# Kernel tuning notes

Measured on AMD Instinct MI355X. Metric: run time of the kernel, lower is better.

## Reference

```python
import jax, jax.numpy as jnp
import numpy as np

DECAY = 0.1
EPS = 1e-5


def setup_inputs() -> dict:
    key = jax.random.key(0)
    k1, k2, k3 = jax.random.split(key, 3)
    H, N, D, K = 1, 32768, 256, 4096
    x = jax.random.normal(k1, (H, N, D), dtype=jnp.float32)
    embed = jax.random.normal(k2, (H, K, D), dtype=jnp.float32) * 0.01
    cluster_size = jnp.ones((H, K), dtype=jnp.float32)
    embed_avg = jax.random.normal(k3, (H, K, D), dtype=jnp.float32) * 0.01
    return {"x": x, "embed": embed, "cluster_size": cluster_size, "embed_avg": embed_avg}


def reference(x, embed, cluster_size, embed_avg):
    # x: [H, N, D] flattened latents; embed: [H, K, D] codebook
    H, N, D = x.shape
    K = embed.shape[1]

    x_sq = jnp.sum(x * x, axis=-1, keepdims=True)          # [H, N, 1]
    e_sq = jnp.sum(embed * embed, axis=-1)[:, None, :]     # [H, 1, K]
    dist = x_sq - 2.0 * jnp.einsum('hnd,hkd->hnk', x, embed) + e_sq

    embed_ind = jnp.argmin(dist, axis=-1)                  # [H, N] int

    # gather nearest code vectors: [H, N, D]
    quantize = jax.vmap(lambda e, i: e[i])(embed, embed_ind)

    # EMA statistics (no_grad in torch): bincount + scatter-add of latents
    bins = jax.vmap(lambda i: jax.ops.segment_sum(jnp.ones((N,), x.dtype), i, num_segments=K))(embed_ind)                      # [H, K]
    embed_sum = jax.vmap(lambda xh, ih: jax.ops.segment_sum(xh, ih, num_segments=K))(x, embed_ind)                             # [H, K, D]

    new_cluster_size = cluster_size * DECAY + bins * (1.0 - DECAY)
    new_embed_avg = embed_avg * DECAY + embed_sum * (1.0 - DECAY)

    # laplace-smoothed normalization of codebook
    n = jnp.sum(new_cluster_size, axis=-1, keepdims=True)
    smoothed = (new_cluster_size + EPS) / (n + K * EPS) * n
    embed_normalized = new_embed_avg / smoothed[..., None]  # [H, K, D]

    # commitment loss (quantize detached) and straight-through output
    commit_loss = jnp.mean((jax.lax.stop_gradient(quantize) - x) ** 2)
    out = x + jax.lax.stop_gradient(quantize - x)

    return out, commit_loss, embed_ind, new_cluster_size, embed_normalized
```

## Files before the change

### kernel.cpp

```cpp
#include <hip/hip_runtime.h>
#include <hip/hip_bf16.h>
#include <cstdint>
#include <cstddef>

#define NROWS 32768
#define DDIM 256
#define KCODES 4096

typedef __attribute__((ext_vector_type(8))) short s16x8;
typedef __attribute__((ext_vector_type(4))) float f32x4;
typedef unsigned long long u64;
typedef unsigned int u32;

#define WS_LOSS 0
#define WS_CNT 1
#define WS_EMAX 2
#define WS_DISTRUST 3
#define WS_NSC 4
#define WS_HIST 8
#define WS_OFFS 4104
#define WS_CURSOR 8200
#define WS_LPART 12296
#define WS_RLIST 16392
#define WS_ESUM 49160
#define WS_XSQ 1097736
#define WS_ESQ 1130504
#define WS_IDX 1134600
#define WS_KEY 1167368
#define WS_TKEY 1232904
#define WS_TM2 1757192
#define WS_LIST 2019336
#define WS_EH 2052104
#define WS_EL 2576392
#define WS_TOTAL 3100680
#define WS_ZERO_FLOATS 12296

__device__ __forceinline__ float hsum16_np(const float a[16]) {
    float t3[8];
#pragma unroll
    for (int m = 0; m < 8; ++m) t3[m] = __fadd_rn(a[m + 8], a[m]);
    float t6[4];
#pragma unroll
    for (int m = 0; m < 4; ++m) t6[m] = __fadd_rn(t3[m + 4], t3[m]);
    return __fadd_rn(__fadd_rn(t6[0], t6[2]), __fadd_rn(t6[1], t6[3]));
}

__device__ __forceinline__ float np_sum_sq_128(const float* a) {
    float t[16];
#pragma unroll
    for (int l = 0; l < 16; ++l) {
        float m0 = __fmul_rn(a[l], a[l]);
        float m1 = __fmul_rn(a[16 + l], a[16 + l]);
        float m2 = __fmul_rn(a[32 + l], a[32 + l]);
        float m3 = __fmul_rn(a[48 + l], a[48 + l]);
        float m4 = __fmul_rn(a[64 + l], a[64 + l]);
        float m5 = __fmul_rn(a[80 + l], a[80 + l]);
        float m6 = __fmul_rn(a[96 + l], a[96 + l]);
        float m7 = __fmul_rn(a[112 + l], a[112 + l]);
        float s01 = __fadd_rn(m0, m1);
        float s23 = __fadd_rn(m2, m3);
        float s45 = __fadd_rn(m4, m5);
        float s67 = __fadd_rn(m6, m7);
        t[l] = __fadd_rn(__fadd_rn(s01, s23), __fadd_rn(s45, s67));
    }
    return hsum16_np(t);
}

__global__ void k_rownorm(const float* __restrict__ src, float* __restrict__ dst, int rows) {
    int r = blockIdx.x * blockDim.x + threadIdx.x;
    if (r < rows) {
        const float* p = src + ((size_t)r << 8);
        dst[r] = __fadd_rn(np_sum_sq_128(p), np_sum_sq_128(p + 128));
    }
}

__global__ void k_emax(const float* __restrict__ esq, float* __restrict__ emax) {
    __shared__ float s[1024];
    int t = threadIdx.x;
    float m = 0.0f;
    for (int i = t; i < KCODES; i += 1024) m = fmaxf(m, esq[i]);
    s[t] = m;
    __syncthreads();
    for (int w = 512; w > 0; w >>= 1) {
        if (t < w) s[t] = fmaxf(s[t], s[t + w]);
        __syncthreads();
    }
    if (t == 0) emax[0] = s[0];
}

__device__ __forceinline__ ushort bf16_rn(float x) {
    u32 u = __float_as_uint(x);
    u32 r = (u + 0x7fffu + ((u >> 16) & 1u)) >> 16;
    return (ushort)r;
}
__device__ __forceinline__ float bf16_f(ushort h) { return __uint_as_float(((u32)h) << 16); }

__global__ void k_pack(const float* __restrict__ src, ushort* __restrict__ hi,
                       ushort* __restrict__ lo) {
    int i = (blockIdx.x * 256 + threadIdx.x) * 8;
    float4 v0 = *reinterpret_cast<const float4*>(src + i);
    float4 v1 = *reinterpret_cast<const float4*>(src + i + 4);
    float f[8] = {v0.x, v0.y, v0.z, v0.w, v1.x, v1.y, v1.z, v1.w};
    ushort h[8], l[8];
#pragma unroll
    for (int j = 0; j < 8; ++j) {
        h[j] = bf16_rn(f[j]);
        l[j] = bf16_rn(__fsub_rn(f[j], bf16_f(h[j])));
    }
    *reinterpret_cast<s16x8*>(hi + i) = *reinterpret_cast<s16x8*>(h);
    *reinterpret_cast<s16x8*>(lo + i) = *reinterpret_cast<s16x8*>(l);
}

__device__ __forceinline__ float keyval_(u64 k) {
    u32 u = (u32)(k >> 32);
    u = (u & 0x80000000u) ? (u ^ 0x80000000u) : ~u;
    return __uint_as_float(u);
}
__device__ __forceinline__ u64 packkey(float d, u32 j) {
    u32 u = __float_as_uint(d);
    u ^= (u32)((int)u >> 31) | 0x80000000u;
    return ((u64)u << 32) | j;
}
#define KEY_INIT 0xFF8000007FFFFFFFull

__device__ __forceinline__ void dma16(const void* g, void* l) {
    __builtin_amdgcn_global_load_lds(
        (const __attribute__((address_space(1))) void*)g,
        (__attribute__((address_space(3))) void*)l, 16, 0, 0);
}

__global__ __attribute__((amdgpu_flat_work_group_size(512, 512), amdgpu_waves_per_eu(4, 4)))
void k_mfma(const ushort* __restrict__ xh_g, const ushort* __restrict__ xl_g,
            const ushort* __restrict__ eh_g, const ushort* __restrict__ el_g,
            const float* __restrict__ xsq, const float* __restrict__ esq,
            u64* __restrict__ tkey, float* __restrict__ tm2) {
    __shared__ __align__(16) ushort xh_s[16384];
    __shared__ __align__(16) ushort xl_s[16384];
    __shared__ __align__(16) ushort eh_s[4096];
    __shared__ __align__(16) ushort el_s[4096];

    const int tid = threadIdx.x;
    const int w = tid >> 6, l = tid & 63, lr = l & 15, lg = l >> 4;
    const int lid = blockIdx.x;
    const int xcd = lid & 7, sslot = lid >> 3, sp = sslot >> 3, ww = sslot & 7;
    const int bxg = xcd * 16 + (sp & 3) * 4 + (ww & 3);
    const int jb = ((sp >> 2) << 1) + (ww >> 2);
    const int n0 = bxg * 256, j0 = jb * 512;
    const int key = (lr & 7) << 4;

    float xq[8];
#pragma unroll
    for (int i = 0; i < 8; ++i)
        xq[i] = xsq[n0 + w * 32 + (i >> 2) * 16 + lg * 4 + (i & 3)];

    u64 K1[8];
    float M2[8];
#pragma unroll
    for (int i = 0; i < 8; ++i) { K1[i] = KEY_INIT; M2[i] = __uint_as_float(0x7F800000u); }

    for (int js = 0; js < 8; ++js) {
        const int jbase = j0 + js * 64;
        f32x4 acc[2][4];
#pragma unroll
        for (int a = 0; a < 2; ++a)
#pragma unroll
            for (int b = 0; b < 4; ++b) acc[a][b] = (f32x4){0.f, 0.f, 0.f, 0.f};

        for (int c = 0; c < 4; ++c) {
            __syncthreads();
#pragma unroll
            for (int p = 0; p < 4; ++p) {
                int m = tid + p * 512, r = m >> 3, cb = (m & 7) << 4;
                int so = (n0 + r) * 256 + c * 64 + ((cb ^ ((r & 7) << 4)) >> 1);
                dma16(xh_g + so, (char*)xh_s + m * 16);
                dma16(xl_g + so, (char*)xl_s + m * 16);
            }
            {
                int m = tid, r = m >> 3, cb = (m & 7) << 4;
                int so = (jbase + r) * 256 + c * 64 + ((cb ^ ((r & 7) << 4)) >> 1);
                dma16(eh_g + so, (char*)eh_s + m * 16);
                dma16(el_g + so, (char*)el_s + m * 16);
            }
            __syncthreads();
#pragma unroll
            for (int ks = 0; ks < 2; ++ks) {
                const int off = (ks * 64 + lg * 16) ^ key;
                s16x8 axh[2], axl[2];
#pragma unroll
                for (int ns = 0; ns < 2; ++ns) {
                    const int row = w * 32 + ns * 16 + lr;
                    axh[ns] = *(const s16x8*)((const char*)(xh_s + row * 64) + off);
                    axl[ns] = *(const s16x8*)((const char*)(xl_s + row * 64) + off);
                }
#pragma unroll
                for (int jp = 0; jp < 2; ++jp) {
                    s16x8 beh[2], bel[2];
#pragma unroll
                    for (int q = 0; q < 2; ++q) {
                        const int row = (jp * 2 + q) * 16 + lr;
                        beh[q] = *(const s16x8*)((const char*)(eh_s + row * 64) + off);
                        bel[q] = *(const s16x8*)((const char*)(el_s + row * 64) + off);
                    }
#pragma unroll
                    for (int q = 0; q < 2; ++q) {
                        const int jsub = jp * 2 + q;
#pragma unroll
                        for (int ns = 0; ns < 2; ++ns) {
                            acc[ns][jsub] = __builtin_amdgcn_mfma_f32_16x16x32_bf16(
                                axh[ns], beh[q], acc[ns][jsub], 0, 0, 0);
                            acc[ns][jsub] = __builtin_amdgcn_mfma_f32_16x16x32_bf16(
                                axh[ns], bel[q], acc[ns][jsub], 0, 0, 0);
                            acc[ns][jsub] = __builtin_amdgcn_mfma_f32_16x16x32_bf16(
                                axl[ns], beh[q], acc[ns][jsub], 0, 0, 0);
                        }
                    }
                }
            }
        }
#pragma unroll
        for (int jsub = 0; jsub < 4; ++jsub) {
            const int j = jbase + jsub * 16 + lr;
            const float eq = esq[j];
#pragma unroll
            for (int ns = 0; ns < 2; ++ns)
#pragma unroll
                for (int r = 0; r < 4; ++r) {
                    const float s = acc[ns][jsub][r];
                    const float d = __fadd_rn(__fsub_rn(xq[ns * 4 + r], __fmul_rn(2.0f, s)), eq);
                    const u64 kk = packkey(d, (u32)j);
                    const int i8 = ns * 4 + r;
                    if (kk < K1[i8]) { M2[i8] = keyval_(K1[i8]); K1[i8] = kk; }
                    else if (d < M2[i8]) M2[i8] = d;
                }
        }
    }
#pragma unroll
    for (int i8 = 0; i8 < 8; ++i8) {
        u64 k1 = K1[i8];
        float m2 = M2[i8];
#pragma unroll
        for (int mk = 1; mk < 16; mk <<= 1) {
            u32 klo = __shfl_xor((u32)k1, mk);
            u32 khi = __shfl_xor((u32)(k1 >> 32), mk);
            float om2 = __shfl_xor(m2, mk);
            u64 ok = ((u64)khi << 32) | klo;
            if (ok < k1) { m2 = fminf(om2, keyval_(k1)); k1 = ok; }
            else m2 = fminf(m2, keyval_(ok));
        }
        if (lr == 0) {
            const int n = n0 + w * 32 + (i8 >> 2) * 16 + lg * 4 + (i8 & 3);
            tkey[(size_t)jb * NROWS + n] = k1;
            tm2[(size_t)jb * NROWS + n] = m2;
        }
    }
}

__global__ void k_merge(const u64* __restrict__ tkey, const float* __restrict__ tm2,
                        const float* __restrict__ xsq, const float* __restrict__ emaxp,
                        u64* __restrict__ key64, u32* __restrict__ list, u32* __restrict__ cnt) {
    const int n = blockIdx.x * 256 + threadIdx.x;
    u64 k1 = tkey[n];
    float m2 = tm2[n];
#pragma unroll
    for (int jb = 1; jb < 8; ++jb) {
        u64 ok = tkey[(size_t)jb * NROWS + n];
        float om2 = tm2[(size_t)jb * NROWS + n];
        if (ok < k1) { m2 = fminf(om2, keyval_(k1)); k1 = ok; }
        else m2 = fminf(m2, keyval_(ok));
    }
    const float B = sqrtf(xsq[n] * emaxp[0]);
    const float Ed = 2.4e-4f * B + 1.5e-4f;
    if (m2 - keyval_(k1) <= 2.0f * Ed) {
        key64[n] = ~0ull;
        list[atomicAdd(cnt, 1u)] = (u32)n;
    } else {
        key64[n] = k1;
    }
}

__global__ void k_verify(const float* __restrict__ x, const float* __restrict__ e,
                         const float* __restrict__ xsq, const float* __restrict__ esq,
                         const float* __restrict__ emaxp, u64* __restrict__ key64,
                         u32* __restrict__ list, u32* __restrict__ cnt,
                         u32* __restrict__ distrust) {
    const int li = threadIdx.x & 15;
    const int n = blockIdx.x * 16 + (threadIdx.x >> 4);
    const u64 k = key64[n];
    const bool active = (k != ~0ull);
    const int idx = active ? (int)(k & 0xFFFu) : 0;
    const float* xr = x + ((size_t)n << 8);
    const float* er = e + ((size_t)idx << 8);
    float a = 0.0f;
#pragma unroll
    for (int g = 0; g < 4; ++g)
#pragma unroll
        for (int bb = 3; bb >= 0; --bb) {
            const int d = (g * 4 + bb) * 16 + li;
            a = __builtin_fmaf(xr[d], er[d], a);
        }
    const float s1 = __fadd_rn(__shfl_xor(a, 8), a);
    const float s2 = __fadd_rn(__shfl_xor(s1, 4), s1);
    const float u = __fadd_rn(s2, __shfl_xor(s2, 2));
    const float dot = __fadd_rn(u, __shfl_xor(u, 1));
    if (li == 0 && active) {
        const float d = __fadd_rn(__fsub_rn(xsq[n], __fmul_rn(2.0f, dot)), esq[idx]);
        const float dref = keyval_(k);
        const float B = sqrtf(xsq[n] * emaxp[0]);
        const float Ed = 2.4e-4f * B + 1.5e-4f;
        const float diff = fabsf(d - dref);
        if (diff > Ed) {
            key64[n] = ~0ull;
            list[atomicAdd(cnt, 1u)] = (u32)n;
            if (diff > 0.05f) atomicOr(distrust, 1u);
        }
    }
}

__global__ void k_distrust(const u32* __restrict__ distrust, u64* __restrict__ key64,
                           u32* __restrict__ list, u32* __restrict__ cnt) {
    if (*distrust == 0u) return;
    const int n = blockIdx.x * 256 + threadIdx.x;
    key64[n] = ~0ull;
    list[n] = (u32)n;
    if (n == 0) *cnt = (u32)NROWS;
}

__global__ __attribute__((amdgpu_flat_work_group_size(512, 512), amdgpu_waves_per_eu(4)))
void k_exact(const float* __restrict__ x, const float* __restrict__ embed,
             const float* __restrict__ xsq, const float* __restrict__ esq,
             const u32* __restrict__ list, const u32* __restrict__ cntp,
             u64* __restrict__ key64) {
    const u32 cnt = *cntp;
    const int grp = blockIdx.x >> 3, seg = blockIdx.x & 7;
    const u32 base = (u32)grp * 32u;
    if (base >= cnt) return;

    __shared__ float xs[32][260];
    __shared__ float es[64][68];
    u64* red = (u64*)&es[0][0];

    const int tid = threadIdx.x;
    const int lane = tid & 63;
    const int w = tid >> 6;
    const int g = w >> 2;
    const int tc = lane & 15;
    const int tr = ((w & 3) << 2) + (lane >> 4);
    const int cbase = (g << 5) + tc;

#pragma unroll
    for (int p = 0; p < 4; ++p) {
        int v = tid + p * 512;
        int r = v >> 6;
        int c4 = (v & 63) << 2;
        u32 row = list[(base + (u32)r < cnt) ? base + r : base];
        const float4 f = *reinterpret_cast<const float4*>(x + ((size_t)row << 8) + c4);
        *reinterpret_cast<float4*>(&xs[r][c4]) = f;
    }

    const u32 row0 = list[(base + (u32)tr < cnt) ? base + tr : base];
    const u32 row1 = list[(base + (u32)tr + 16u < cnt) ? base + tr + 16 : base];
    const float xq0 = xsq[row0];
    const float xq1 = xsq[row1];

    u64 best0 = ~0ull, best1 = ~0ull;

    for (int ktl = 0; ktl < 8; ++ktl) {
        const int k0 = seg * 512 + ktl * 64;
        float acc[2][2][16];
#pragma unroll
        for (int i = 0; i < 2; ++i)
#pragma unroll
            for (int j = 0; j < 2; ++j)
#pragma unroll
                for (int q = 0; q < 16; ++q) acc[i][j][q] = 0.0f;

        for (int c = 0; c < 4; ++c) {
            __syncthreads();
#pragma unroll
            for (int p = 0; p < 2; ++p) {
                int v = tid + p * 512;
                int r = v >> 4;
                int c4 = (v & 15) << 2;
                const float4 f = *reinterpret_cast<const float4*>(
                    embed + ((size_t)(k0 + r) << 8) + (c << 6) + c4);
                *reinterpret_cast<float4*>(&es[r][c4]) = f;
            }
            __syncthreads();
#pragma unroll
            for (int jj = 3; jj >= 0; --jj) {
#pragma unroll
                for (int q = 0; q < 4; ++q) {
                    const int dl = ((c * 4 + jj) << 4) + (q << 2);
                    const int el = (jj << 4) + (q << 2);
                    const float4 a0 = *reinterpret_cast<const float4*>(&xs[tr][dl]);
                    const float4 a1 = *reinterpret_cast<const float4*>(&xs[tr + 16][dl]);
                    const int lb = q << 2;
#pragma unroll
                    for (int j2 = 0; j2 < 2; ++j2) {
                        const float4 b = *reinterpret_cast<const float4*>(&es[cbase + 16 * j2][el]);
                        acc[0][j2][lb + 0] = __builtin_fmaf(a0.x, b.x, acc[0][j2][lb + 0]);
                        acc[0][j2][lb + 1] = __builtin_fmaf(a0.y, b.y, acc[0][j2][lb + 1]);
                        acc[0][j2][lb + 2] = __builtin_fmaf(a0.z, b.z, acc[0][j2][lb + 2]);
                        acc[0][j2][lb + 3] = __builtin_fmaf(a0.w, b.w, acc[0][j2][lb + 3]);
                        acc[1][j2][lb + 0] = __builtin_fmaf(a1.x, b.x, acc[1][j2][lb + 0]);
                        acc[1][j2][lb + 1] = __builtin_fmaf(a1.y, b.y, acc[1][j2][lb + 1]);
                        acc[1][j2][lb + 2] = __builtin_fmaf(a1.z, b.z, acc[1][j2][lb + 2]);
                        acc[1][j2][lb + 3] = __builtin_fmaf(a1.w, b.w, acc[1][j2][lb + 3]);
                    }
                }
            }
        }
#pragma unroll
        for (int j2 = 0; j2 < 2; ++j2) {
            const int kk = k0 + cbase + 16 * j2;
            const float eq = esq[kk];
            {
                const float dist = __fadd_rn(__fsub_rn(xq0, __fmul_rn(2.0f, hsum16_np(acc[0][j2]))), eq);
                const u64 kkey = packkey(dist, (u32)kk);
                best0 = kkey < best0 ? kkey : best0;
            }
            {
                const float dist = __fadd_rn(__fsub_rn(xq1, __fmul_rn(2.0f, hsum16_np(acc[1][j2]))), eq);
                const u64 kkey = packkey(dist, (u32)kk);
                best1 = kkey < best1 ? kkey : best1;
            }
        }
    }

    __syncthreads();
    red[tr * 32 + (g << 4) + tc] = best0;
    red[(tr + 16) * 32 + (g << 4) + tc] = best1;
    __syncthreads();
    if (tid < 32) {
        u64 m = red[tid * 32];
#pragma unroll
        for (int t = 1; t < 32; ++t) {
            u64 v = red[tid * 32 + t];
            m = v < m ? v : m;
        }
        if (base + (u32)tid < cnt) atomicMin(&key64[list[base + tid]], m);
    }
}

__global__ void k_finhist(const u64* __restrict__ key64, int* __restrict__ idx,
                          u32* __restrict__ hist, float* __restrict__ ind_out) {
    const int n = blockIdx.x * 256 + threadIdx.x;
    const int k = (int)(key64[n] & 0xFFFull);
    idx[n] = k;
    atomicAdd(&hist[k], 1u);
    ind_out[n] = (float)k;
}

__global__ void k_histidx(const int* __restrict__ idx, u32* __restrict__ hist,
                          float* __restrict__ ind_out) {
    const int n = blockIdx.x * 256 + threadIdx.x;
    const int k = idx[n];
    atomicAdd(&hist[k], 1u);
    ind_out[n] = (float)k;
}

__global__ __attribute__((amdgpu_flat_work_group_size(512, 512), amdgpu_waves_per_eu(4)))
void k_argmin_full(const float* __restrict__ x, const float* __restrict__ embed,
                   const float* __restrict__ xsq, const float* __restrict__ esq,
                   int* __restrict__ out_idx) {
    __shared__ float xs[32][260];
    __shared__ float es[64][68];
    u64* red = (u64*)&es[0][0];
    const int tid = threadIdx.x;
    const int lane = tid & 63;
    const int w = tid >> 6;
    const int g = w >> 2;
    const int tc = lane & 15;
    const int tr = ((w & 3) << 2) + (lane >> 4);
    const int cbase = (g << 5) + tc;
    const int n0 = blockIdx.x * 32;
#pragma unroll
    for (int p = 0; p < 4; ++p) {
        int v = tid + p * 512;
        int r = v >> 6;
        int c4 = (v & 63) << 2;
        const float4 f = *reinterpret_cast<const float4*>(x + ((size_t)(n0 + r) << 8) + c4);
        *reinterpret_cast<float4*>(&xs[r][c4]) = f;
    }
    const float xq0 = xsq[n0 + tr];
    const float xq1 = xsq[n0 + tr + 16];
    u64 best0 = ~0ull, best1 = ~0ull;
    for (int kt = 0; kt < KCODES / 64; ++kt) {
        const int k0 = kt * 64;
        float acc[2][2][16];
#pragma unroll
        for (int i = 0; i < 2; ++i)
#pragma unroll
            for (int j = 0; j < 2; ++j)
#pragma unroll
                for (int q = 0; q < 16; ++q) acc[i][j][q] = 0.0f;
        for (int c = 0; c < 4; ++c) {
            __syncthreads();
#pragma unroll
            for (int p = 0; p < 2; ++p) {
                int v = tid + p * 512;
                int r = v >> 4;
                int c4 = (v & 15) << 2;
                const float4 f = *reinterpret_cast<const float4*>(
                    embed + ((size_t)(k0 + r) << 8) + (c << 6) + c4);
                *reinterpret_cast<float4*>(&es[r][c4]) = f;
            }
            __syncthreads();
#pragma unroll
            for (int jj = 3; jj >= 0; --jj) {
#pragma unroll
                for (int q = 0; q < 4; ++q) {
                    const int dl = ((c * 4 + jj) << 4) + (q << 2);
                    const int el = (jj << 4) + (q << 2);
                    const float4 a0 = *reinterpret_cast<const float4*>(&xs[tr][dl]);
                    const float4 a1 = *reinterpret_cast<const float4*>(&xs[tr + 16][dl]);
                    const int lb = q << 2;
#pragma unroll
                    for (int j2 = 0; j2 < 2; ++j2) {
                        const float4 b = *reinterpret_cast<const float4*>(&es[cbase + 16 * j2][el]);
                        acc[0][j2][lb + 0] = __builtin_fmaf(a0.x, b.x, acc[0][j2][lb + 0]);
                        acc[0][j2][lb + 1] = __builtin_fmaf(a0.y, b.y, acc[0][j2][lb + 1]);
                        acc[0][j2][lb + 2] = __builtin_fmaf(a0.z, b.z, acc[0][j2][lb + 2]);
                        acc[0][j2][lb + 3] = __builtin_fmaf(a0.w, b.w, acc[0][j2][lb + 3]);
                        acc[1][j2][lb + 0] = __builtin_fmaf(a1.x, b.x, acc[1][j2][lb + 0]);
                        acc[1][j2][lb + 1] = __builtin_fmaf(a1.y, b.y, acc[1][j2][lb + 1]);
                        acc[1][j2][lb + 2] = __builtin_fmaf(a1.z, b.z, acc[1][j2][lb + 2]);
                        acc[1][j2][lb + 3] = __builtin_fmaf(a1.w, b.w, acc[1][j2][lb + 3]);
                    }
                }
            }
        }
#pragma unroll
        for (int j2 = 0; j2 < 2; ++j2) {
            const int kk = k0 + cbase + 16 * j2;
            const float eq = esq[kk];
            {
                const float dist = __fadd_rn(__fsub_rn(xq0, __fmul_rn(2.0f, hsum16_np(acc[0][j2]))), eq);
                const u64 kkey = packkey(dist, (u32)kk);
                best0 = kkey < best0 ? kkey : best0;
            }
            {
                const float dist = __fadd_rn(__fsub_rn(xq1, __fmul_rn(2.0f, hsum16_np(acc[1][j2]))), eq);
                const u64 kkey = packkey(dist, (u32)kk);
                best1 = kkey < best1 ? kkey : best1;
            }
        }
    }
    __syncthreads();
    red[tr * 32 + (g << 4) + tc] = best0;
    red[(tr + 16) * 32 + (g << 4) + tc] = best1;
    __syncthreads();
    if (tid < 32) {
        u64 m = red[tid * 32];
#pragma unroll
        for (int t = 1; t < 32; ++t) {
            u64 v = red[tid * 32 + t];
            m = v < m ? v : m;
        }
        out_idx[n0 + tid] = (int)(m & 0xFFFFFFFFu);
    }
}

__global__ void k_scancluster(const u32* __restrict__ hist, u32* __restrict__ offs,
                              const float* __restrict__ cs, float* __restrict__ ncs_out,
                              float* __restrict__ n_out) {
    __shared__ u32 ts[1024];
    __shared__ float fs[1024];
    const int t = threadIdx.x;
    const u32 h0 = hist[t * 4], h1 = hist[t * 4 + 1], h2 = hist[t * 4 + 2], h3 = hist[t * 4 + 3];
    const u32 tot = h0 + h1 + h2 + h3;
    ts[t] = tot;
    const float n0_ = __fadd_rn(__fmul_rn(cs[t * 4 + 0], 0.1f), __fmul_rn((float)h0, 0.9f));
    const float n1_ = __fadd_rn(__fmul_rn(cs[t * 4 + 1], 0.1f), __fmul_rn((float)h1, 0.9f));
    const float n2_ = __fadd_rn(__fmul_rn(cs[t * 4 + 2], 0.1f), __fmul_rn((float)h2, 0.9f));
    const float n3_ = __fadd_rn(__fmul_rn(cs[t * 4 + 3], 0.1f), __fmul_rn((float)h3, 0.9f));
    ncs_out[t * 4 + 0] = n0_;
    ncs_out[t * 4 + 1] = n1_;
    ncs_out[t * 4 + 2] = n2_;
    ncs_out[t * 4 + 3] = n3_;
    fs[t] = ((n0_ + n1_) + n2_) + n3_;
    __syncthreads();
    for (int o = 1; o < 1024; o <<= 1) {
        const u32 add = (t >= o) ? ts[t - o] : 0u;
        __syncthreads();
        ts[t] += add;
        __syncthreads();
    }
    const u32 excl = ts[t] - tot;
    offs[t * 4] = excl;
    offs[t * 4 + 1] = excl + h0;
    offs[t * 4 + 2] = excl + h0 + h1;
    offs[t * 4 + 3] = excl + h0 + h1 + h2;
    for (int wd = 512; wd > 0; wd >>= 1) {
        if (t < wd) fs[t] += fs[t + wd];
        __syncthreads();
    }
    if (t == 0) n_out[0] = fs[0];
}

__global__ void k_place(const int* __restrict__ idx, u32* __restrict__ cursor,
                        const u32* __restrict__ offs, u32* __restrict__ rlist) {
    const int n = blockIdx.x * 256 + threadIdx.x;
    const int k = idx[n];
    const u32 p = atomicAdd(&cursor[k], 1u);
    rlist[offs[k] + p] = (u32)n;
}

__global__ void k_esum(const float* __restrict__ x, const u32* __restrict__ rlist,
                       const u32* __restrict__ offs, const u32* __restrict__ hist,
                       float* __restrict__ esum) {
    const int k = blockIdx.x;
    const int d = threadIdx.x;
    const u32 o = offs[k], c = hist[k];
    float s = 0.0f;
    for (u32 i = 0; i < c; ++i) s += x[((size_t)rlist[o + i] << 8) + d];
    esum[((size_t)k << 8) + d] = s;
}

__global__ void k_outloss(const float* __restrict__ x, const float* __restrict__ e,
                          const int* __restrict__ idx, float* __restrict__ out,
                          float* __restrict__ lpart) {
    const int d = threadIdx.x;
    float ls = 0.0f;
#pragma unroll
    for (int r = 0; r < 8; ++r) {
        const int n = blockIdx.x * 8 + r;
        const int k = idx[n];
        const size_t xi = ((size_t)n << 8) + d;
        const float xv = x[xi];
        const float qv = e[((size_t)k << 8) + d];
        const float diff = __fsub_rn(qv, xv);
        out[xi] = __fadd_rn(xv, diff);
        ls = __builtin_fmaf(diff, diff, ls);
    }
    __shared__ float sred[256];
    sred[d] = ls;
    __syncthreads();
    for (int s = 128; s > 0; s >>= 1) {
        if (d < s) sred[d] += sred[d + s];
        __syncthreads();
    }
    if (d == 0) lpart[blockIdx.x] = sred[0];
}

__global__ void k_norm(const float* __restrict__ ea, const float* __restrict__ esum,
                       const float* __restrict__ ncs, const float* __restrict__ nptr,
                       float* __restrict__ en_out) {
    const int i = blockIdx.x * 256 + threadIdx.x;
    const int k = i >> 8;
    const float n = nptr[0];
    const float ncsk = ncs[k];
    const float smoothed = (ncsk + 1e-5f) / (n + 4096.0f * 1e-5f) * n;
    const float nea = __fadd_rn(__fmul_rn(ea[i], 0.1f), __fmul_rn(esum[i], 0.9f));
    en_out[i] = nea / smoothed;
}

__global__ void k_loss(const float* __restrict__ lpart, float* __restrict__ dst) {
    __shared__ float s[256];
    const int t = threadIdx.x;
    float a = 0.0f;
    for (int i = t; i < 4096; i += 256) a += lpart[i];
    s[t] = a;
    __syncthreads();
    for (int w = 128; w > 0; w >>= 1) {
        if (t < w) s[t] += s[t + w];
        __syncthreads();
    }
    if (t == 0) dst[0] = s[0] * (1.0f / 8388608.0f);
}

extern "C" void kernel_launch(void* const* d_in, const int* in_sizes, int n_in, void* d_out,
                              int out_size, void* d_ws, size_t ws_size, hipStream_t stream) {
    (void)in_sizes; (void)n_in; (void)out_size;
    const float* x = (const float*)d_in[0];
    const float* emb = (const float*)d_in[1];
    const float* cs = (const float*)d_in[2];
    const float* ea = (const float*)d_in[3];
    float* ws = (float*)d_ws;
    float* out = (float*)d_out;

    u32* w_cnt = (u32*)(ws + WS_CNT);
    float* w_emax = ws + WS_EMAX;
    u32* w_dis = (u32*)(ws + WS_DISTRUST);
    float* w_n = ws + WS_NSC;
    u32* w_hist = (u32*)(ws + WS_HIST);
    u32* w_offs = (u32*)(ws + WS_OFFS);
    u32* w_cursor = (u32*)(ws + WS_CURSOR);
    float* w_lpart = ws + WS_LPART;
    u32* w_rlist = (u32*)(ws + WS_RLIST);
    float* w_esum = ws + WS_ESUM;
    float* w_xsq = ws + WS_XSQ;
    float* w_esq = ws + WS_ESQ;
    int* w_idx = (int*)(ws + WS_IDX);
    u64* w_key = (u64*)(ws + WS_KEY);
    u64* w_tkey = (u64*)(ws + WS_TKEY);
    float* w_tm2 = ws + WS_TM2;
    u32* w_list = (u32*)(ws + WS_LIST);
    ushort* eh_g = (ushort*)(ws + WS_EH);
    ushort* el_g = (ushort*)(ws + WS_EL);

    float* o_out = out;
    float* o_loss = out + 8388608;
    float* o_ind = out + 8388609;
    float* o_ncs = out + 8421377;
    float* o_en = out + 8425473;

    ushort* xh_g = (ushort*)o_out;
    ushort* xl_g = (ushort*)o_out + 8388608;

    hipMemsetAsync(d_ws, 0, (size_t)WS_ZERO_FLOATS * sizeof(float), stream);

    k_rownorm<<<NROWS / 256, 256, 0, stream>>>(x, w_xsq, NROWS);
    k_rownorm<<<KCODES / 256, 256, 0, stream>>>(emb, w_esq, KCODES);

    if (ws_size >= (size_t)WS_TOTAL * sizeof(float)) {
        k_emax<<<1, 1024, 0, stream>>>(w_esq, w_emax);
        k_pack<<<4096, 256, 0, stream>>>(x, xh_g, xl_g);
        k_pack<<<512, 256, 0, stream>>>(emb, eh_g, el_g);
        k_mfma<<<1024, 512, 0, stream>>>(xh_g, xl_g, eh_g, el_g, w_xsq, w_esq,
                                         w_tkey, w_tm2);
        k_merge<<<128, 256, 0, stream>>>(w_tkey, w_tm2, w_xsq, w_emax, w_key, w_list, w_cnt);
        k_verify<<<2048, 256, 0, stream>>>(x, emb, w_xsq, w_esq, w_emax, w_key, w_list,
                                           w_cnt, w_dis);
        k_distrust<<<128, 256, 0, stream>>>(w_dis, w_key, w_list, w_cnt);
        k_exact<<<8192, 512, 0, stream>>>(x, emb, w_xsq, w_esq, w_list, w_cnt, w_key);
        k_finhist<<<128, 256, 0, stream>>>(w_key, w_idx, w_hist, o_ind);
    } else {
        k_argmin_full<<<NROWS / 32, 512, 0, stream>>>(x, emb, w_xsq, w_esq, w_idx);
        k_histidx<<<128, 256, 0, stream>>>(w_idx, w_hist, o_ind);
    }

    k_scancluster<<<1, 1024, 0, stream>>>(w_hist, w_offs, cs, o_ncs, w_n);
    k_place<<<128, 256, 0, stream>>>(w_idx, w_cursor, w_offs, w_rlist);
    k_esum<<<KCODES, 256, 0, stream>>>(x, w_rlist, w_offs, w_hist, w_esum);
    k_outloss<<<NROWS / 8, 256, 0, stream>>>(x, emb, w_idx, o_out, w_lpart);
    k_norm<<<(KCODES * DDIM) / 256, 256, 0, stream>>>(ea, w_esum, o_ncs, w_n, o_en);
    k_loss<<<1, 256, 0, stream>>>(w_lpart, o_loss);
}
```

Measured before the change: 448.2 us.

## Fuse row norms into bf16 packing and esum with normalization; simplify MFMA grid

Row-norm computation is folded into the bf16 hi/lo packing kernel. The codebook max norm is now taken with an atomicMax on the float bits inside that kernel, so the separate rownorm and emax launches go away. Embed-sum accumulation is fused with the EMA/laplace normalization, so the intermediate esum array is neither written nor re-read. The MFMA launch drops its XCD-aware block swizzle for a plain 2D grid, which may change L2 locality across XCDs.

```diff
diff --git a/kernel.cpp b/kernel.cpp
--- a/kernel.cpp
+++ b/kernel.cpp
@@ -32,7 +32,7 @@
 #define WS_LIST 2019336
 #define WS_EH 2052104
 #define WS_EL 2576392
-#define WS_TOTAL 3100680
+#define WS_TOTAL 3055624
 #define WS_ZERO_FLOATS 12296
 
 __device__ __forceinline__ float hsum16_np(const float a[16]) {
@@ -74,20 +74,6 @@
     }
 }
 
-__global__ void k_emax(const float* __restrict__ esq, float* __restrict__ emax) {
-    __shared__ float s[1024];
-    int t = threadIdx.x;
-    float m = 0.0f;
-    for (int i = t; i < KCODES; i += 1024) m = fmaxf(m, esq[i]);
-    s[t] = m;
-    __syncthreads();
-    for (int w = 512; w > 0; w >>= 1) {
-        if (t < w) s[t] = fmaxf(s[t], s[t + w]);
-        __syncthreads();
-    }
-    if (t == 0) emax[0] = s[0];
-}
-
 __device__ __forceinline__ ushort bf16_rn(float x) {
     u32 u = __float_as_uint(x);
     u32 r = (u + 0x7fffu + ((u >> 16) & 1u)) >> 16;
@@ -95,20 +81,41 @@
 }
 __device__ __forceinline__ float bf16_f(ushort h) { return __uint_as_float(((u32)h) << 16); }
 
-__global__ void k_pack(const float* __restrict__ src, ushort* __restrict__ hi,
-                       ushort* __restrict__ lo) {
-    int i = (blockIdx.x * 256 + threadIdx.x) * 8;
-    float4 v0 = *reinterpret_cast<const float4*>(src + i);
-    float4 v1 = *reinterpret_cast<const float4*>(src + i + 4);
+__global__ void k_packnorm(const float* __restrict__ src, ushort* __restrict__ hi,
+                           ushort* __restrict__ lo, float* __restrict__ dst,
+                           u32* __restrict__ emax_u32) {
+    __shared__ float lf[8][257];
+    __shared__ float lsq[8];
+    const int t = threadIdx.x;
+    const int r8 = t >> 5, c8 = (t & 31) << 3;
+    const size_t base = ((size_t)(blockIdx.x * 8 + r8) << 8) + c8;
+    float4 v0 = *reinterpret_cast<const float4*>(src + base);
+    float4 v1 = *reinterpret_cast<const float4*>(src + base + 4);
     float f[8] = {v0.x, v0.y, v0.z, v0.w, v1.x, v1.y, v1.z, v1.w};
     ushort h[8], l[8];
 #pragma unroll
     for (int j = 0; j < 8; ++j) {
         h[j] = bf16_rn(f[j]);
         l[j] = bf16_rn(__fsub_rn(f[j], bf16_f(h[j])));
-    }
-    *reinterpret_cast<s16x8*>(hi + i) = *reinterpret_cast<s16x8*>(h);
-    *reinterpret_cast<s16x8*>(lo + i) = *reinterpret_cast<s16x8*>(l);
+        lf[r8][c8 + j] = f[j];
+    }
+    *reinterpret_cast<s16x8*>(hi + base) = *reinterpret_cast<s16x8*>(h);
+    *reinterpret_cast<s16x8*>(lo + base) = *reinterpret_cast<s16x8*>(l);
+    __syncthreads();
+    if (t < 8) {
+        const float sq = __fadd_rn(np_sum_sq_128(&lf[t][0]), np_sum_sq_128(&lf[t][128]));
+        dst[blockIdx.x * 8 + t] = sq;
+        lsq[t] = sq;
+    }
+    if (emax_u32) {
+        __syncthreads();
+        if (t == 0) {
+            float m = lsq[0];
+#pragma unroll
+            for (int i = 1; i < 8; ++i) m = fmaxf(m, lsq[i]);
+            atomicMax(emax_u32, __float_as_uint(m));
+        }
+    }
 }
 
 __device__ __forceinline__ float keyval_(u64 k) {
@@ -141,11 +148,7 @@
 
     const int tid = threadIdx.x;
     const int w = tid >> 6, l = tid & 63, lr = l & 15, lg = l >> 4;
-    const int lid = blockIdx.x;
-    const int xcd = lid & 7, sslot = lid >> 3, sp = sslot >> 3, ww = sslot & 7;
-    const int bxg = xcd * 16 + (sp & 3) * 4 + (ww & 3);
-    const int jb = ((sp >> 2) << 1) + (ww >> 2);
-    const int n0 = bxg * 256, j0 = jb * 512;
+    const int n0 = blockIdx.x * 256, jb = blockIdx.y, j0 = jb * 512;
     const int key = (lr & 7) << 4;
 
     float xq[8];
@@ -606,15 +609,21 @@
     rlist[offs[k] + p] = (u32)n;
 }
 
-__global__ void k_esum(const float* __restrict__ x, const u32* __restrict__ rlist,
-                       const u32* __restrict__ offs, const u32* __restrict__ hist,
-                       float* __restrict__ esum) {
+__global__ void k_esumnorm(const float* __restrict__ x, const u32* __restrict__ rlist,
+                           const u32* __restrict__ offs, const u32* __restrict__ hist,
+                           const float* __restrict__ ea, const float* __restrict__ ncs,
+                           const float* __restrict__ nptr, float* __restrict__ en_out) {
     const int k = blockIdx.x;
     const int d = threadIdx.x;
     const u32 o = offs[k], c = hist[k];
     float s = 0.0f;
     for (u32 i = 0; i < c; ++i) s += x[((size_t)rlist[o + i] << 8) + d];
-    esum[((size_t)k << 8) + d] = s;
+    const float n = nptr[0];
+    const float ncsk = ncs[k];
+    const float smoothed = (ncsk + 1e-5f) / (n + 4096.0f * 1e-5f) * n;
+    const size_t ix = ((size_t)k << 8) + d;
+    const float nea = __fadd_rn(__fmul_rn(ea[ix], 0.1f), __fmul_rn(s, 0.9f));
+    en_out[ix] = nea / smoothed;
 }
 
 __global__ void k_outloss(const float* __restrict__ x, const float* __restrict__ e,
@@ -653,6 +662,17 @@
     const float smoothed = (ncsk + 1e-5f) / (n + 4096.0f * 1e-5f) * n;
     const float nea = __fadd_rn(__fmul_rn(ea[i], 0.1f), __fmul_rn(esum[i], 0.9f));
     en_out[i] = nea / smoothed;
+}
+
+__global__ void k_esum(const float* __restrict__ x, const u32* __restrict__ rlist,
+                       const u32* __restrict__ offs, const u32* __restrict__ hist,
+                       float* __restrict__ esum) {
+    const int k = blockIdx.x;
+    const int d = threadIdx.x;
+    const u32 o = offs[k], c = hist[k];
+    float s = 0.0f;
+    for (u32 i = 0; i < c; ++i) s += x[((size_t)rlist[o + i] << 8) + d];
+    esum[((size_t)k << 8) + d] = s;
 }
 
 __global__ void k_loss(const float* __restrict__ lpart, float* __restrict__ dst) {
@@ -710,30 +730,32 @@
 
     hipMemsetAsync(d_ws, 0, (size_t)WS_ZERO_FLOATS * sizeof(float), stream);
 
-    k_rownorm<<<NROWS / 256, 256, 0, stream>>>(x, w_xsq, NROWS);
-    k_rownorm<<<KCODES / 256, 256, 0, stream>>>(emb, w_esq, KCODES);
-
     if (ws_size >= (size_t)WS_TOTAL * sizeof(float)) {
-        k_emax<<<1, 1024, 0, stream>>>(w_esq, w_emax);
-        k_pack<<<4096, 256, 0, stream>>>(x, xh_g, xl_g);
-        k_pack<<<512, 256, 0, stream>>>(emb, eh_g, el_g);
-        k_mfma<<<1024, 512, 0, stream>>>(xh_g, xl_g, eh_g, el_g, w_xsq, w_esq,
-                                         w_tkey, w_tm2);
+        k_packnorm<<<NROWS / 8, 256, 0, stream>>>(x, xh_g, xl_g, w_xsq, nullptr);
+        k_packnorm<<<KCODES / 8, 256, 0, stream>>>(emb, eh_g, el_g, w_esq, (u32*)w_emax);
+        k_mfma<<<dim3(128, 8), 512, 0, stream>>>(xh_g, xl_g, eh_g, el_g, w_xsq, w_esq,
+                                                 w_tkey, w_tm2);
         k_merge<<<128, 256, 0, stream>>>(w_tkey, w_tm2, w_xsq, w_emax, w_key, w_list, w_cnt);
         k_verify<<<2048, 256, 0, stream>>>(x, emb, w_xsq, w_esq, w_emax, w_key, w_list,
                                            w_cnt, w_dis);
         k_distrust<<<128, 256, 0, stream>>>(w_dis, w_key, w_list, w_cnt);
         k_exact<<<8192, 512, 0, stream>>>(x, emb, w_xsq, w_esq, w_list, w_cnt, w_key);
         k_finhist<<<128, 256, 0, stream>>>(w_key, w_idx, w_hist, o_ind);
+        k_scancluster<<<1, 1024, 0, stream>>>(w_hist, w_offs, cs, o_ncs, w_n);
+        k_place<<<128, 256, 0, stream>>>(w_idx, w_cursor, w_offs, w_rlist);
+        k_esumnorm<<<KCODES, 256, 0, stream>>>(x, w_rlist, w_offs, w_hist, ea, o_ncs, w_n, o_en);
+        k_outloss<<<NROWS / 8, 256, 0, stream>>>(x, emb, w_idx, o_out, w_lpart);
+        k_loss<<<1, 256, 0, stream>>>(w_lpart, o_loss);
     } else {
+        k_rownorm<<<NROWS / 256, 256, 0, stream>>>(x, w_xsq, NROWS);
+        k_rownorm<<<KCODES / 256, 256, 0, stream>>>(emb, w_esq, KCODES);
         k_argmin_full<<<NROWS / 32, 512, 0, stream>>>(x, emb, w_xsq, w_esq, w_idx);
         k_histidx<<<128, 256, 0, stream>>>(w_idx, w_hist, o_ind);
-    }
-
-    k_scancluster<<<1, 1024, 0, stream>>>(w_hist, w_offs, cs, o_ncs, w_n);
-    k_place<<<128, 256, 0, stream>>>(w_idx, w_cursor, w_offs, w_rlist);
-    k_esum<<<KCODES, 256, 0, stream>>>(x, w_rlist, w_offs, w_hist, w_esum);
-    k_outloss<<<NROWS / 8, 256, 0, stream>>>(x, emb, w_idx, o_out, w_lpart);
-    k_norm<<<(KCODES * DDIM) / 256, 256, 0, stream>>>(ea, w_esum, o_ncs, w_n, o_en);
-    k_loss<<<1, 256, 0, stream>>>(w_lpart, o_loss);
-}
+        k_scancluster<<<1, 1024, 0, stream>>>(w_hist, w_offs, cs, o_ncs, w_n);
+        k_place<<<128, 256, 0, stream>>>(w_idx, w_cursor, w_offs, w_rlist);
+        k_esum<<<KCODES, 256, 0, stream>>>(x, w_rlist, w_offs, w_hist, w_esum);
+        k_outloss<<<NROWS / 8, 256, 0, stream>>>(x, emb, w_idx, o_out, w_lpart);
+        k_norm<<<(KCODES * DDIM) / 256, 256, 0, stream>>>(ea, w_esum, o_ncs, w_n, o_en);
+        k_loss<<<1, 256, 0, stream>>>(w_lpart, o_loss);
+    }
+}
```

Measured after the change: 407.4 us (median of 2 runs). 9.1% less time.
